# Kernel tuning notes

Measured on AMD Instinct MI355X. Metric: run time of the kernel, lower is better.

The kernel has to match this reference:

```python
import jax, jax.numpy as jnp
import numpy as np
from jax import lax


def _na_indices(size, k):
    # NATTEN-style window: window shifts to stay inside the volume.
    centers = np.arange(size)
    start = np.clip(centers - k // 2, 0, size - k)
    idx = start[:, None] + np.arange(k)[None, :]          # (size, k) neighbor coords
    rel = idx - centers[:, None] + (k - 1)                # (size, k) in [0, 2k-2]
    return jnp.asarray(idx), jnp.asarray(rel)


def _ln(x, g, b):
    mu = jnp.mean(x, axis=-1, keepdims=True)
    var = jnp.mean(jnp.square(x - mu), axis=-1, keepdims=True)
    return (x - mu) * lax.rsqrt(var + 1e-5) * g + b


def setup_inputs() -> dict:
    key = jax.random.key(0)
    ks = jax.random.split(key, 12)
    B, C, H, W, Z = 1, 128, 64, 64, 8
    heads, k = 8, 3
    s = lambda kk, shp: (jax.random.normal(kk, shp, jnp.float32) * 0.02)
    return {
        "x": jax.random.normal(ks[0], (B, C, H, W, Z), jnp.float32),
        "ln1_g": jnp.ones((C,), jnp.float32), "ln1_b": jnp.zeros((C,), jnp.float32),
        "qkv_w": s(ks[1], (C, 3 * C)), "qkv_b": jnp.zeros((3 * C,), jnp.float32),
        "proj_w": s(ks[2], (C, C)), "proj_b": jnp.zeros((C,), jnp.float32),
        "rpb": s(ks[3], (heads, 2 * k - 1, 2 * k - 1, 2 * k - 1)),
        "ln2_g": jnp.ones((C,), jnp.float32), "ln2_b": jnp.zeros((C,), jnp.float32),
        "w1": s(ks[4], (C, 4 * C)), "b1": jnp.zeros((4 * C,), jnp.float32),
        "w2": s(ks[5], (4 * C, C)), "b2": jnp.zeros((C,), jnp.float32),
    }


def reference(x, ln1_g, ln1_b, qkv_w, qkv_b, proj_w, proj_b, rpb,
              ln2_g, ln2_b, w1, b1, w2, b2):
    B, C, H, W, Z = x.shape
    heads = rpb.shape[0]
    k = (rpb.shape[1] + 1) // 2
    hd = C // heads
    K3 = k * k * k

    xp = jnp.transpose(x, (0, 2, 3, 4, 1))                 # (B,H,W,Z,C)
    res1 = xp
    xn = _ln(xp, ln1_g, ln1_b)
    qkv = xn @ qkv_w + qkv_b
    q, kk, v = jnp.split(qkv, 3, axis=-1)

    ih, rh = _na_indices(H, k)
    iw, rw = _na_indices(W, k)
    iz, rz = _na_indices(Z, k)
    Ih = ih[:, None, None, :, None, None]
    Iw = iw[None, :, None, None, :, None]
    Iz = iz[None, None, :, None, None, :]
    # gathered neighborhoods: (B,H,W,Z,k,k,k,C) -> (B,H,W,Z,K3,heads,hd)
    k_n = kk[:, Ih, Iw, Iz, :].reshape(B, H, W, Z, K3, heads, hd)
    v_n = v[:, Ih, Iw, Iz, :].reshape(B, H, W, Z, K3, heads, hd)
    qh = q.reshape(B, H, W, Z, heads, hd) * (hd ** -0.5)

    # scores: (B,H,W,Z,heads,K3)
    scores = jnp.einsum('bxyzne,bxyzmne->bxyznm', qh, k_n)
    bias = rpb[:, rh[:, None, None, :, None, None],
                  rw[None, :, None, None, :, None],
                  rz[None, None, :, None, None, :]]        # (heads,H,W,Z,k,k,k)
    bias = bias.reshape(heads, H, W, Z, K3).transpose(1, 2, 3, 0, 4)
    attn = jax.nn.softmax(scores + bias[None], axis=-1)

    out = jnp.einsum('bxyznm,bxyzmne->bxyzne', attn, v_n).reshape(B, H, W, Z, C)
    out = out @ proj_w + proj_b
    x1 = res1 + out                                        # attention residual
    h = jax.nn.gelu(_ln(x1, ln2_g, ln2_b) @ w1 + b1) @ w2 + b2
    x2 = x1 + h                                            # FFN residual

    enc = jnp.transpose(x2, (0, 4, 1, 2, 3))               # (B,C,H,W,Z)
    skip = enc + x                                         # outer residual
    pooled = lax.reduce_window(skip, -jnp.inf, lax.max,
                               (1, 1, 2, 2, 2), (1, 1, 2, 2, 2), 'VALID')
    return (pooled, skip)
```

## Files before the change

### kernel.cpp

```cpp
#include <hip/hip_runtime.h>
#include <hip/hip_bf16.h>
#include <math.h>

#define NPOS 32768

typedef __hip_bfloat16 bf16;
typedef __attribute__((ext_vector_type(8))) short bf16x8;
typedef __attribute__((ext_vector_type(4))) float f32x4;

__device__ __forceinline__ float bf2f(short s) {
    union { unsigned u; float f; } cv;
    cv.u = ((unsigned)(unsigned short)s) << 16;
    return cv.f;
}

__global__ __launch_bounds__(256) void wt_transpose_kernel(
    const float* __restrict__ src, bf16* __restrict__ dst, int K, int M)
{
    __shared__ float tile[32][33];
    int m0 = blockIdx.x * 32, k0 = blockIdx.y * 32;
    int tx = threadIdx.x & 31, ty = threadIdx.x >> 5;
    #pragma unroll
    for (int i = 0; i < 4; i++)
        tile[ty + i * 8][tx] = src[(size_t)(k0 + ty + i * 8) * M + m0 + tx];
    __syncthreads();
    #pragma unroll
    for (int i = 0; i < 4; i++)
        dst[(size_t)(m0 + ty + i * 8) * K + k0 + tx] = __float2bfloat16(tile[tx][ty + i * 8]);
}

__global__ __launch_bounds__(256) void ln1_transpose_kernel(
    const float* __restrict__ x, const float* __restrict__ g,
    const float* __restrict__ b, bf16* __restrict__ out)
{
    __shared__ float tile[128][65];
    __shared__ float red[2][64][4];
    __shared__ float smu[64], srs[64];
    int n0 = blockIdx.x * 64;
    int tid = threadIdx.x;
    #pragma unroll
    for (int i = 0; i < 32; i++) {
        int idx = i * 256 + tid;
        int c = idx >> 6, nn = idx & 63;
        tile[c][nn] = x[(size_t)c * NPOS + n0 + nn];
    }
    __syncthreads();
    {
        int p = tid >> 2, s = tid & 3;
        float sum = 0.f, ssq = 0.f;
        #pragma unroll
        for (int i = 0; i < 32; i++) {
            float v = tile[s * 32 + i][p];
            sum += v; ssq += v * v;
        }
        red[0][p][s] = sum; red[1][p][s] = ssq;
    }
    __syncthreads();
    if (tid < 64) {
        float s = red[0][tid][0] + red[0][tid][1] + red[0][tid][2] + red[0][tid][3];
        float q = red[1][tid][0] + red[1][tid][1] + red[1][tid][2] + red[1][tid][3];
        float mu = s * (1.f / 128.f);
        float var = q * (1.f / 128.f) - mu * mu;
        smu[tid] = mu;
        srs[tid] = rsqrtf(var + 1e-5f);
    }
    __syncthreads();
    #pragma unroll
    for (int i = 0; i < 32; i++) {
        int idx = i * 256 + tid;
        int nn = idx >> 7, c = idx & 127;
        out[(size_t)(n0 + nn) * 128 + c] =
            __float2bfloat16((tile[c][nn] - smu[nn]) * srs[nn] * g[c] + b[c]);
    }
}

__device__ __forceinline__ float gelu_f(float v) {
    float t = tanhf(0.7978845608028654f * (v + 0.044715f * v * v * v));
    return 0.5f * v * (1.f + t);
}

template<int MODE>
__global__ __launch_bounds__(256) void gemm_mfma_kernel(
    const bf16* __restrict__ A, const bf16* __restrict__ Bt,
    const float* __restrict__ bias, void* __restrict__ outv,
    const float* __restrict__ aux0, const float* __restrict__ aux1,
    int N, int K, int M)
{
    __shared__ __align__(16) bf16 As[128][72];
    __shared__ __align__(16) bf16 Bs[128][72];
    int tid = threadIdx.x;
    int row0 = blockIdx.x * 128;
    int col0 = blockIdx.y * 128;
    int lane = tid & 63, wid = tid >> 6;
    int wr = wid >> 1, wc = wid & 1;
    int lr = lane & 15, kg = lane >> 4;

    f32x4 acc[4][4] = {};

    for (int k0 = 0; k0 < K; k0 += 64) {
        bf16x8 ra[4], rb[4];
        #pragma unroll
        for (int i = 0; i < 4; i++) {
            int c = tid + i * 256;
            int r = c >> 3, c8 = c & 7;
            ra[i] = *(const bf16x8*)(A  + (size_t)(row0 + r) * K + k0 + c8 * 8);
            rb[i] = *(const bf16x8*)(Bt + (size_t)(col0 + r) * K + k0 + c8 * 8);
        }
        if (k0 > 0) __syncthreads();
        #pragma unroll
        for (int i = 0; i < 4; i++) {
            int c = tid + i * 256;
            int r = c >> 3, c8 = c & 7;
            *(bf16x8*)&As[r][c8 * 8] = ra[i];
            *(bf16x8*)&Bs[r][c8 * 8] = rb[i];
        }
        __syncthreads();
        #pragma unroll
        for (int ks = 0; ks < 2; ks++) {
            bf16x8 af[4], bf_[4];
            #pragma unroll
            for (int m = 0; m < 4; m++)
                af[m] = *(const bf16x8*)&As[wr * 64 + m * 16 + lr][ks * 32 + kg * 8];
            #pragma unroll
            for (int n = 0; n < 4; n++)
                bf_[n] = *(const bf16x8*)&Bs[wc * 64 + n * 16 + lr][ks * 32 + kg * 8];
            #pragma unroll
            for (int m = 0; m < 4; m++)
                #pragma unroll
                for (int n = 0; n < 4; n++)
                    acc[m][n] = __builtin_amdgcn_mfma_f32_16x16x32_bf16(af[m], bf_[n], acc[m][n], 0, 0, 0);
        }
    }

    #pragma unroll
    for (int m = 0; m < 4; m++) {
        #pragma unroll
        for (int n = 0; n < 4; n++) {
            int c = col0 + wc * 64 + n * 16 + lr;
            float bv = bias[c];
            #pragma unroll
            for (int j = 0; j < 4; j++) {
                int r = row0 + wr * 64 + m * 16 + kg * 4 + j;
                float v = acc[m][n][j] + bv;
                if (MODE == 0) {
                    ((bf16*)outv)[(size_t)r * M + c] = __float2bfloat16(v);
                } else if (MODE == 1) {
                    v += aux0[(size_t)c * N + r];
                    ((float*)outv)[(size_t)r * M + c] = v;
                } else if (MODE == 2) {
                    ((bf16*)outv)[(size_t)r * M + c] = __float2bfloat16(gelu_f(v));
                } else {
                    v += aux1[(size_t)r * 128 + c] + aux0[(size_t)c * N + r];
                    ((float*)outv)[(size_t)c * N + r] = v;
                }
            }
        }
    }
}

__global__ __launch_bounds__(256) void attn_kernel(
    const bf16* __restrict__ qkv,
    const float* __restrict__ rpb,
    bf16* __restrict__ out)
{
    __shared__ __align__(16) bf16 klds[144 * 136];
    __shared__ __align__(16) bf16 vlds[144 * 136];
    int tid = threadIdx.x;
    int h  = blockIdx.x >> 4;
    int w0 = (blockIdx.x & 15) << 2;
    int n0 = (h << 9) + (w0 << 3);
    int bh = min(max(h - 1, 0), 61);
    int bw = min(max(w0 - 1, 0), 58);

    #pragma unroll
    for (int i = 0; i < 18; i++) {
        int chunk = i * 256 + tid;
        int s = chunk >> 5;
        int w32 = chunk & 31;
        int isv = w32 >> 4, c16 = w32 & 15;
        unsigned rc = (unsigned)(s >> 3);
        int z = s & 7;
        int r = rc / 6u, c = rc % 6u;
        int ns = ((bh + r) << 9) + ((bw + c) << 3) + z;
        bf16x8 val = *(const bf16x8*)(qkv + (size_t)ns * 384 + 128 + isv * 128 + c16 * 8);
        bf16* dst = (isv ? vlds : klds) + s * 136 + c16 * 8;
        *(bf16x8*)dst = val;
    }
    __syncthreads();

    int p = tid >> 3, head = tid & 7;
    int pw = p >> 3, z = p & 7;
    int w = w0 + pw;
    int n = n0 + p;

    float qf[16];
    {
        const bf16* qp = qkv + (size_t)n * 384 + head * 16;
        bf16x8 q0 = *(const bf16x8*)qp;
        bf16x8 q1 = *(const bf16x8*)(qp + 8);
        #pragma unroll
        for (int e = 0; e < 8; e++) {
            qf[e]     = bf2f(q0[e]) * 0.25f;
            qf[e + 8] = bf2f(q1[e]) * 0.25f;
        }
    }

    int sw = min(max(w - 1, 0), 61);
    int sz = min(max(z - 1, 0), 5);
    int cb = sw - bw;

    float sc[27];
    int   lp[27];
    float mx = -1e30f;
    int mi = 0;
    #pragma unroll
    for (int a = 0; a < 3; a++) {
        #pragma unroll
        for (int b = 0; b < 3; b++) {
            #pragma unroll
            for (int c = 0; c < 3; c++) {
                int lpos = ((a * 6 + cb + b) << 3) + sz + c;
                const bf16* kp = klds + lpos * 136 + head * 16;
                bf16x8 k0 = *(const bf16x8*)kp;
                bf16x8 k1 = *(const bf16x8*)(kp + 8);
                float s = 0.f;
                #pragma unroll
                for (int e = 0; e < 8; e++) s = fmaf(qf[e], bf2f(k0[e]), s);
                #pragma unroll
                for (int e = 0; e < 8; e++) s = fmaf(qf[e + 8], bf2f(k1[e]), s);
                s += rpb[head * 125 + (bh + a - h + 2) * 25 + (sw + b - w + 2) * 5 + (sz + c - z + 2)];
                sc[mi] = s;
                lp[mi] = lpos;
                mx = fmaxf(mx, s);
                mi++;
            }
        }
    }

    float sum = 0.f;
    #pragma unroll
    for (int m = 0; m < 27; m++) {
        float e = __expf(sc[m] - mx);
        sc[m] = e;
        sum += e;
    }
    float inv = 1.f / sum;

    float o[16] = {};
    #pragma unroll
    for (int m = 0; m < 27; m++) {
        const bf16* vp = vlds + lp[m] * 136 + head * 16;
        bf16x8 v0 = *(const bf16x8*)vp;
        bf16x8 v1 = *(const bf16x8*)(vp + 8);
        float pm = sc[m];
        #pragma unroll
        for (int e = 0; e < 8; e++) {
            o[e]     = fmaf(pm, bf2f(v0[e]), o[e]);
            o[e + 8] = fmaf(pm, bf2f(v1[e]), o[e + 8]);
        }
    }

    bf16* op = out + (size_t)n * 128 + head * 16;
    #pragma unroll
    for (int e = 0; e < 16; e++)
        op[e] = __float2bfloat16(o[e] * inv);
}

__global__ __launch_bounds__(256) void ln_rows_kernel(
    const float* __restrict__ in, const float* __restrict__ g,
    const float* __restrict__ b, bf16* __restrict__ out)
{
    int wid = (blockIdx.x * 256 + threadIdx.x) >> 6;
    int lane = threadIdx.x & 63;
    if (wid >= NPOS) return;
    const float* row = in + (size_t)wid * 128;
    float v0 = row[lane], v1 = row[lane + 64];
    float s = v0 + v1, ss = v0 * v0 + v1 * v1;
    #pragma unroll
    for (int o = 32; o > 0; o >>= 1) { s += __shfl_down(s, o); ss += __shfl_down(ss, o); }
    s = __shfl(s, 0); ss = __shfl(ss, 0);
    float mu = s * (1.f / 128.f);
    float var = ss * (1.f / 128.f) - mu * mu;
    float rs = rsqrtf(var + 1e-5f);
    out[(size_t)wid * 128 + lane]      = __float2bfloat16((v0 - mu) * rs * g[lane] + b[lane]);
    out[(size_t)wid * 128 + lane + 64] = __float2bfloat16((v1 - mu) * rs * g[lane + 64] + b[lane + 64]);
}

__global__ __launch_bounds__(256) void pool_kernel(
    const float* __restrict__ skip, float* __restrict__ pooled)
{
    int t = blockIdx.x * 256 + threadIdx.x;
    if (t >= 128 * 32 * 32 * 4) return;
    int oz = t & 3, ow = (t >> 2) & 31, oh = (t >> 7) & 31, c = t >> 12;
    const float* base = skip + (size_t)c * 32768 + (oh * 2) * 512 + (ow * 2) * 8 + oz * 2;
    float m = -INFINITY;
    #pragma unroll
    for (int dh = 0; dh < 2; dh++)
        #pragma unroll
        for (int dw = 0; dw < 2; dw++)
            #pragma unroll
            for (int dz = 0; dz < 2; dz++)
                m = fmaxf(m, base[dh * 512 + dw * 8 + dz]);
    pooled[t] = m;
}

extern "C" void kernel_launch(void* const* d_in, const int* in_sizes, int n_in,
                              void* d_out, int out_size, void* d_ws, size_t ws_size,
                              hipStream_t stream) {
    const float* x      = (const float*)d_in[0];
    const float* ln1_g  = (const float*)d_in[1];
    const float* ln1_b  = (const float*)d_in[2];
    const float* qkv_w  = (const float*)d_in[3];
    const float* qkv_b  = (const float*)d_in[4];
    const float* proj_w = (const float*)d_in[5];
    const float* proj_b = (const float*)d_in[6];
    const float* rpb    = (const float*)d_in[7];
    const float* ln2_g  = (const float*)d_in[8];
    const float* ln2_b  = (const float*)d_in[9];
    const float* w1     = (const float*)d_in[10];
    const float* b1     = (const float*)d_in[11];
    const float* w2     = (const float*)d_in[12];
    const float* b2     = (const float*)d_in[13];

    const int N = NPOS;
    char* wsc = (char*)d_ws;
    bf16*  buf0 = (bf16*)wsc;
    bf16*  buf1 = (bf16*)(wsc + (size_t)N * 128 * 2);
    float* buf2 = (float*)(wsc + (size_t)N * 128 * 2 + (size_t)N * 512 * 2);
    char*  wts  = wsc + (size_t)N * 128 * 2 + (size_t)N * 512 * 2 + (size_t)N * 128 * 4;
    bf16* wt_qkv  = (bf16*)wts;
    bf16* wt_proj = wt_qkv  + 384 * 128;
    bf16* wt_w1   = wt_proj + 128 * 128;
    bf16* wt_w2   = wt_w1   + 512 * 128;

    float* out_pooled = (float*)d_out;
    float* out_skip   = (float*)d_out + 524288;

    wt_transpose_kernel<<<dim3(384 / 32, 128 / 32), 256, 0, stream>>>(qkv_w, wt_qkv, 128, 384);
    wt_transpose_kernel<<<dim3(128 / 32, 128 / 32), 256, 0, stream>>>(proj_w, wt_proj, 128, 128);
    wt_transpose_kernel<<<dim3(512 / 32, 128 / 32), 256, 0, stream>>>(w1, wt_w1, 128, 512);
    wt_transpose_kernel<<<dim3(128 / 32, 512 / 32), 256, 0, stream>>>(w2, wt_w2, 512, 128);

    ln1_transpose_kernel<<<N / 64, 256, 0, stream>>>(x, ln1_g, ln1_b, buf0);

    gemm_mfma_kernel<0><<<dim3(N / 128, 384 / 128), 256, 0, stream>>>(
        buf0, wt_qkv, qkv_b, buf1, nullptr, nullptr, N, 128, 384);

    attn_kernel<<<1024, 256, 0, stream>>>(buf1, rpb, buf0);

    gemm_mfma_kernel<1><<<dim3(N / 128, 1), 256, 0, stream>>>(
        buf0, wt_proj, proj_b, buf2, x, nullptr, N, 128, 128);

    ln_rows_kernel<<<N / 4, 256, 0, stream>>>(buf2, ln2_g, ln2_b, buf0);

    gemm_mfma_kernel<2><<<dim3(N / 128, 512 / 128), 256, 0, stream>>>(
        buf0, wt_w1, b1, buf1, nullptr, nullptr, N, 128, 512);

    gemm_mfma_kernel<3><<<dim3(N / 128, 1), 256, 0, stream>>>(
        buf1, wt_w2, b2, out_skip, x, buf2, N, 512, 128);

    pool_kernel<<<(524288 + 255) / 256, 256, 0, stream>>>(out_skip, out_pooled);
}
```

Before: 207.4 us.

## Fuse LN2 into proj GEMM, merge weight prep, widen GEMM K tile

```diff
diff --git a/kernel.cpp b/kernel.cpp
--- a/kernel.cpp
+++ b/kernel.cpp
@@ -14,11 +14,21 @@
     return cv.f;
 }
 
-__global__ __launch_bounds__(256) void wt_transpose_kernel(
-    const float* __restrict__ src, bf16* __restrict__ dst, int K, int M)
+__global__ __launch_bounds__(256) void prep_weights_kernel(
+    const float* __restrict__ qkv_w, const float* __restrict__ proj_w,
+    const float* __restrict__ w1, const float* __restrict__ w2,
+    bf16* __restrict__ wt_qkv, bf16* __restrict__ wt_proj,
+    bf16* __restrict__ wt_w1, bf16* __restrict__ wt_w2)
 {
+    int bi = blockIdx.x;
+    const float* src; bf16* dst; int K, M, t;
+    if (bi < 48)       { src = qkv_w;  dst = wt_qkv;  K = 128; M = 384; t = bi; }
+    else if (bi < 64)  { src = proj_w; dst = wt_proj; K = 128; M = 128; t = bi - 48; }
+    else if (bi < 128) { src = w1;     dst = wt_w1;   K = 128; M = 512; t = bi - 64; }
+    else               { src = w2;     dst = wt_w2;   K = 512; M = 128; t = bi - 128; }
+    int tiles_x = M >> 5;
+    int m0 = (t % tiles_x) * 32, k0 = (t / tiles_x) * 32;
     __shared__ float tile[32][33];
-    int m0 = blockIdx.x * 32, k0 = blockIdx.y * 32;
     int tx = threadIdx.x & 31, ty = threadIdx.x >> 5;
     #pragma unroll
     for (int i = 0; i < 4; i++)
@@ -82,12 +92,15 @@
 template<int MODE>
 __global__ __launch_bounds__(256) void gemm_mfma_kernel(
     const bf16* __restrict__ A, const bf16* __restrict__ Bt,
-    const float* __restrict__ bias, void* __restrict__ outv,
+    const float* __restrict__ bias, float* __restrict__ outf, bf16* __restrict__ outb,
     const float* __restrict__ aux0, const float* __restrict__ aux1,
+    const float* __restrict__ lng, const float* __restrict__ lnb,
     int N, int K, int M)
 {
-    __shared__ __align__(16) bf16 As[128][72];
-    __shared__ __align__(16) bf16 Bs[128][72];
+    __shared__ __align__(16) char smem[69632];
+    bf16 (*As)[136] = (bf16(*)[136])smem;
+    bf16 (*Bs)[136] = (bf16(*)[136])(smem + 34816);
+
     int tid = threadIdx.x;
     int row0 = blockIdx.x * 128;
     int col0 = blockIdx.y * 128;
@@ -97,26 +110,26 @@
 
     f32x4 acc[4][4] = {};
 
-    for (int k0 = 0; k0 < K; k0 += 64) {
-        bf16x8 ra[4], rb[4];
-        #pragma unroll
-        for (int i = 0; i < 4; i++) {
-            int c = tid + i * 256;
-            int r = c >> 3, c8 = c & 7;
-            ra[i] = *(const bf16x8*)(A  + (size_t)(row0 + r) * K + k0 + c8 * 8);
-            rb[i] = *(const bf16x8*)(Bt + (size_t)(col0 + r) * K + k0 + c8 * 8);
+    for (int k0 = 0; k0 < K; k0 += 128) {
+        bf16x8 ra[8], rb[8];
+        #pragma unroll
+        for (int i = 0; i < 8; i++) {
+            int q = i * 256 + tid;
+            int r = q >> 4, c16 = q & 15;
+            ra[i] = *(const bf16x8*)(A  + (size_t)(row0 + r) * K + k0 + c16 * 8);
+            rb[i] = *(const bf16x8*)(Bt + (size_t)(col0 + r) * K + k0 + c16 * 8);
         }
         if (k0 > 0) __syncthreads();
         #pragma unroll
-        for (int i = 0; i < 4; i++) {
-            int c = tid + i * 256;
-            int r = c >> 3, c8 = c & 7;
-            *(bf16x8*)&As[r][c8 * 8] = ra[i];
-            *(bf16x8*)&Bs[r][c8 * 8] = rb[i];
+        for (int i = 0; i < 8; i++) {
+            int q = i * 256 + tid;
+            int r = q >> 4, c16 = q & 15;
+            *(bf16x8*)&As[r][c16 * 8] = ra[i];
+            *(bf16x8*)&Bs[r][c16 * 8] = rb[i];
         }
         __syncthreads();
         #pragma unroll
-        for (int ks = 0; ks < 2; ks++) {
+        for (int ks = 0; ks < 4; ks++) {
             bf16x8 af[4], bf_[4];
             #pragma unroll
             for (int m = 0; m < 4; m++)
@@ -132,26 +145,77 @@
         }
     }
 
-    #pragma unroll
-    for (int m = 0; m < 4; m++) {
-        #pragma unroll
-        for (int n = 0; n < 4; n++) {
-            int c = col0 + wc * 64 + n * 16 + lr;
-            float bv = bias[c];
+    if (MODE == 0 || MODE == 2 || MODE == 3) {
+        #pragma unroll
+        for (int m = 0; m < 4; m++) {
+            #pragma unroll
+            for (int n = 0; n < 4; n++) {
+                int c = col0 + wc * 64 + n * 16 + lr;
+                float bv = bias[c];
+                #pragma unroll
+                for (int j = 0; j < 4; j++) {
+                    int r = row0 + wr * 64 + m * 16 + kg * 4 + j;
+                    float v = acc[m][n][j] + bv;
+                    if (MODE == 0) {
+                        outb[(size_t)r * M + c] = __float2bfloat16(v);
+                    } else if (MODE == 2) {
+                        outb[(size_t)r * M + c] = __float2bfloat16(gelu_f(v));
+                    } else {
+                        v += aux1[(size_t)r * 128 + c] + aux0[(size_t)c * N + r];
+                        outf[(size_t)c * N + r] = v;
+                    }
+                }
+            }
+        }
+    } else {
+        __syncthreads();
+        float (*rsum)[33] = (float(*)[33])smem;
+        float (*rsq)[33]  = (float(*)[33])(smem + 16896);
+        float* smu = (float*)(smem + 33792);
+        float* srs = (float*)(smem + 34304);
+        int slot = wc * 16 + lr;
+        #pragma unroll
+        for (int m = 0; m < 4; m++) {
             #pragma unroll
             for (int j = 0; j < 4; j++) {
-                int r = row0 + wr * 64 + m * 16 + kg * 4 + j;
-                float v = acc[m][n][j] + bv;
-                if (MODE == 0) {
-                    ((bf16*)outv)[(size_t)r * M + c] = __float2bfloat16(v);
-                } else if (MODE == 1) {
-                    v += aux0[(size_t)c * N + r];
-                    ((float*)outv)[(size_t)r * M + c] = v;
-                } else if (MODE == 2) {
-                    ((bf16*)outv)[(size_t)r * M + c] = __float2bfloat16(gelu_f(v));
-                } else {
-                    v += aux1[(size_t)r * 128 + c] + aux0[(size_t)c * N + r];
-                    ((float*)outv)[(size_t)c * N + r] = v;
+                int rloc = wr * 64 + m * 16 + kg * 4 + j;
+                int r = row0 + rloc;
+                float ps = 0.f, pq = 0.f;
+                #pragma unroll
+                for (int n = 0; n < 4; n++) {
+                    int c = wc * 64 + n * 16 + lr;
+                    float v = acc[m][n][j] + bias[c] + aux0[(size_t)c * N + r];
+                    acc[m][n][j] = v;
+                    outf[(size_t)r * 128 + c] = v;
+                    ps += v; pq += v * v;
+                }
+                rsum[rloc][slot] = ps;
+                rsq[rloc][slot]  = pq;
+            }
+        }
+        __syncthreads();
+        if (tid < 128) {
+            float s = 0.f, q = 0.f;
+            #pragma unroll
+            for (int i = 0; i < 32; i++) { s += rsum[tid][i]; q += rsq[tid][i]; }
+            float mu = s * (1.f / 128.f);
+            float var = q * (1.f / 128.f) - mu * mu;
+            smu[tid] = mu;
+            srs[tid] = rsqrtf(var + 1e-5f);
+        }
+        __syncthreads();
+        #pragma unroll
+        for (int m = 0; m < 4; m++) {
+            #pragma unroll
+            for (int j = 0; j < 4; j++) {
+                int rloc = wr * 64 + m * 16 + kg * 4 + j;
+                int r = row0 + rloc;
+                float mu = smu[rloc], rs = srs[rloc];
+                #pragma unroll
+                for (int n = 0; n < 4; n++) {
+                    int c = wc * 64 + n * 16 + lr;
+                    float v = (acc[m][n][j] - mu) * rs * lng[c] + lnb[c];
+                    outb[(size_t)r * 128 + c] = __float2bfloat16(v);
                 }
             }
         }
@@ -163,8 +227,9 @@
     const float* __restrict__ rpb,
     bf16* __restrict__ out)
 {
-    __shared__ __align__(16) bf16 klds[144 * 136];
-    __shared__ __align__(16) bf16 vlds[144 * 136];
+    __shared__ __align__(16) bf16 klds[144 * 134];
+    __shared__ __align__(16) bf16 vlds[144 * 134];
+    __shared__ float srpb[1000];
     int tid = threadIdx.x;
     int h  = blockIdx.x >> 4;
     int w0 = (blockIdx.x & 15) << 2;
@@ -172,6 +237,11 @@
     int bh = min(max(h - 1, 0), 61);
     int bw = min(max(w0 - 1, 0), 58);
 
+    #pragma unroll
+    for (int i = 0; i < 4; i++) {
+        int idx = i * 256 + tid;
+        if (idx < 1000) srpb[idx] = rpb[idx];
+    }
     #pragma unroll
     for (int i = 0; i < 18; i++) {
         int chunk = i * 256 + tid;
@@ -183,7 +253,7 @@
         int r = rc / 6u, c = rc % 6u;
         int ns = ((bh + r) << 9) + ((bw + c) << 3) + z;
         bf16x8 val = *(const bf16x8*)(qkv + (size_t)ns * 384 + 128 + isv * 128 + c16 * 8);
-        bf16* dst = (isv ? vlds : klds) + s * 136 + c16 * 8;
+        bf16* dst = (isv ? vlds : klds) + s * 134 + c16 * 8;
         *(bf16x8*)dst = val;
     }
     __syncthreads();
@@ -220,7 +290,7 @@
             #pragma unroll
             for (int c = 0; c < 3; c++) {
                 int lpos = ((a * 6 + cb + b) << 3) + sz + c;
-                const bf16* kp = klds + lpos * 136 + head * 16;
+                const bf16* kp = klds + lpos * 134 + head * 16;
                 bf16x8 k0 = *(const bf16x8*)kp;
                 bf16x8 k1 = *(const bf16x8*)(kp + 8);
                 float s = 0.f;
@@ -228,7 +298,7 @@
                 for (int e = 0; e < 8; e++) s = fmaf(qf[e], bf2f(k0[e]), s);
                 #pragma unroll
                 for (int e = 0; e < 8; e++) s = fmaf(qf[e + 8], bf2f(k1[e]), s);
-                s += rpb[head * 125 + (bh + a - h + 2) * 25 + (sw + b - w + 2) * 5 + (sz + c - z + 2)];
+                s += srpb[head * 125 + (bh + a - h + 2) * 25 + (sw + b - w + 2) * 5 + (sz + c - z + 2)];
                 sc[mi] = s;
                 lp[mi] = lpos;
                 mx = fmaxf(mx, s);
@@ -249,7 +319,7 @@
     float o[16] = {};
     #pragma unroll
     for (int m = 0; m < 27; m++) {
-        const bf16* vp = vlds + lp[m] * 136 + head * 16;
+        const bf16* vp = vlds + lp[m] * 134 + head * 16;
         bf16x8 v0 = *(const bf16x8*)vp;
         bf16x8 v1 = *(const bf16x8*)(vp + 8);
         float pm = sc[m];
@@ -264,26 +334,6 @@
     #pragma unroll
     for (int e = 0; e < 16; e++)
         op[e] = __float2bfloat16(o[e] * inv);
-}
-
-__global__ __launch_bounds__(256) void ln_rows_kernel(
-    const float* __restrict__ in, const float* __restrict__ g,
-    const float* __restrict__ b, bf16* __restrict__ out)
-{
-    int wid = (blockIdx.x * 256 + threadIdx.x) >> 6;
-    int lane = threadIdx.x & 63;
-    if (wid >= NPOS) return;
-    const float* row = in + (size_t)wid * 128;
-    float v0 = row[lane], v1 = row[lane + 64];
-    float s = v0 + v1, ss = v0 * v0 + v1 * v1;
-    #pragma unroll
-    for (int o = 32; o > 0; o >>= 1) { s += __shfl_down(s, o); ss += __shfl_down(ss, o); }
-    s = __shfl(s, 0); ss = __shfl(ss, 0);
-    float mu = s * (1.f / 128.f);
-    float var = ss * (1.f / 128.f) - mu * mu;
-    float rs = rsqrtf(var + 1e-5f);
-    out[(size_t)wid * 128 + lane]      = __float2bfloat16((v0 - mu) * rs * g[lane] + b[lane]);
-    out[(size_t)wid * 128 + lane + 64] = __float2bfloat16((v1 - mu) * rs * g[lane + 64] + b[lane + 64]);
 }
 
 __global__ __launch_bounds__(256) void pool_kernel(
@@ -336,28 +386,24 @@
     float* out_pooled = (float*)d_out;
     float* out_skip   = (float*)d_out + 524288;
 
-    wt_transpose_kernel<<<dim3(384 / 32, 128 / 32), 256, 0, stream>>>(qkv_w, wt_qkv, 128, 384);
-    wt_transpose_kernel<<<dim3(128 / 32, 128 / 32), 256, 0, stream>>>(proj_w, wt_proj, 128, 128);
-    wt_transpose_kernel<<<dim3(512 / 32, 128 / 32), 256, 0, stream>>>(w1, wt_w1, 128, 512);
-    wt_transpose_kernel<<<dim3(128 / 32, 512 / 32), 256, 0, stream>>>(w2, wt_w2, 512, 128);
+    prep_weights_kernel<<<192, 256, 0, stream>>>(qkv_w, proj_w, w1, w2,
+                                                 wt_qkv, wt_proj, wt_w1, wt_w2);
 
     ln1_transpose_kernel<<<N / 64, 256, 0, stream>>>(x, ln1_g, ln1_b, buf0);
 
-    gemm_mfma_kernel<0><<<dim3(N / 128, 384 / 128), 256, 0, stream>>>(
-        buf0, wt_qkv, qkv_b, buf1, nullptr, nullptr, N, 128, 384);
+    gemm_mfma_kernel<0><<<dim3(N / 128, 3), 256, 0, stream>>>(
+        buf0, wt_qkv, qkv_b, nullptr, buf1, nullptr, nullptr, nullptr, nullptr, N, 128, 384);
 
     attn_kernel<<<1024, 256, 0, stream>>>(buf1, rpb, buf0);
 
-    gemm_mfma_kernel<1><<<dim3(N / 128, 1), 256, 0, stream>>>(
-        buf0, wt_proj, proj_b, buf2, x, nullptr, N, 128, 128);
-
-    ln_rows_kernel<<<N / 4, 256, 0, stream>>>(buf2, ln2_g, ln2_b, buf0);
-
-    gemm_mfma_kernel<2><<<dim3(N / 128, 512 / 128), 256, 0, stream>>>(
-        buf0, wt_w1, b1, buf1, nullptr, nullptr, N, 128, 512);
+    gemm_mfma_kernel<4><<<dim3(N / 128, 1), 256, 0, stream>>>(
+        buf0, wt_proj, proj_b, buf2, buf0, x, nullptr, ln2_g, ln2_b, N, 128, 128);
+
+    gemm_mfma_kernel<2><<<dim3(N / 128, 4), 256, 0, stream>>>(
+        buf0, wt_w1, b1, nullptr, buf1, nullptr, nullptr, nullptr, nullptr, N, 128, 512);
 
     gemm_mfma_kernel<3><<<dim3(N / 128, 1), 256, 0, stream>>>(
-        buf1, wt_w2, b2, out_skip, x, buf2, N, 512, 128);
+        buf1, wt_w2, b2, out_skip, nullptr, x, buf2, nullptr, nullptr, N, 512, 128);
 
     pool_kernel<<<(524288 + 255) / 256, 256, 0, stream>>>(out_skip, out_pooled);
 }
```

After: 230.1 us. 10.9% more time.
